# Kernel optimization log

Measured on AMD Instinct MI355X. Metric: run time of the kernel, lower is better.

Reference implementation:

```python
import jax, jax.numpy as jnp
import numpy as np

H = 1024  # hidden_size

def _lstm_cell(x, h, c, Wih, Whh, bih, bhh):
    # x:[B,in], h/c:[B,H]; PyTorch gate order i,f,g,o
    g = x @ Wih.T + h @ Whh.T + (bih + bhh)
    i, f, gg, o = jnp.split(g, 4, axis=-1)
    c = jax.nn.sigmoid(f) * c + jax.nn.sigmoid(i) * jnp.tanh(gg)
    h = jax.nn.sigmoid(o) * jnp.tanh(c)
    return h, c

def setup_inputs() -> dict:
    key = jax.random.key(0)
    ks = jax.random.split(key, 24)
    s = 0.05
    def W(k, shape):
        return (jax.random.normal(k, shape, dtype=jnp.float32) * s)
    inp = {
        'prev': jax.random.normal(ks[0], (32, 256), dtype=jnp.float32),
        'n': jax.random.normal(ks[1], (32, 256), dtype=jnp.float32),
        'tf_mask': jax.random.bernoulli(ks[2], 0.5, (256,)),
        # encoder layer 0 (input_size=1) and layer 1 (input_size=H)
        'enc_Wih0': W(ks[3], (4*H, 1)),  'enc_Whh0': W(ks[4], (4*H, H)),
        'enc_bih0': W(ks[5], (4*H,)),    'enc_bhh0': W(ks[6], (4*H,)),
        'enc_Wih1': W(ks[7], (4*H, H)),  'enc_Whh1': W(ks[8], (4*H, H)),
        'enc_bih1': W(ks[9], (4*H,)),    'enc_bhh1': W(ks[10], (4*H,)),
        # decoder layers
        'dec_Wih0': W(ks[11], (4*H, 1)), 'dec_Whh0': W(ks[12], (4*H, H)),
        'dec_bih0': W(ks[13], (4*H,)),   'dec_bhh0': W(ks[14], (4*H,)),
        'dec_Wih1': W(ks[15], (4*H, H)), 'dec_Whh1': W(ks[16], (4*H, H)),
        'dec_bih1': W(ks[17], (4*H,)),   'dec_bhh1': W(ks[18], (4*H,)),
        'fc_w': W(ks[19], (1, H)),       'fc_b': W(ks[20], (1,)),
    }
    return inp

def reference(prev, n, tf_mask,
              enc_Wih0, enc_Whh0, enc_bih0, enc_bhh0,
              enc_Wih1, enc_Whh1, enc_bih1, enc_bhh1,
              dec_Wih0, dec_Whh0, dec_bih0, dec_bhh0,
              dec_Wih1, dec_Whh1, dec_bih1, dec_bhh1,
              fc_w, fc_b):
    B = prev.shape[0]
    z = jnp.zeros((B, H), dtype=prev.dtype)

    # ---- encode: scan over timesteps, scalar input per step ----
    def enc_step(carry, x_t):
        h0, c0, h1, c1 = carry
        x = x_t[:, None]  # [B,1]
        h0, c0 = _lstm_cell(x, h0, c0, enc_Wih0, enc_Whh0, enc_bih0, enc_bhh0)
        h1, c1 = _lstm_cell(h0, h1, c1, enc_Wih1, enc_Whh1, enc_bih1, enc_bhh1)
        return (h0, c0, h1, c1), None

    carry, _ = jax.lax.scan(enc_step, (z, z, z, z), prev.T)  # prev.T: [T,B]

    # ---- decode with teacher forcing mask ----
    def dec_step(carry, inputs):
        h0, c0, h1, c1, x = carry
        n_t, tf = inputs
        h0, c0 = _lstm_cell(x, h0, c0, dec_Wih0, dec_Whh0, dec_bih0, dec_bhh0)
        h1, c1 = _lstm_cell(h0, h1, c1, dec_Wih1, dec_Whh1, dec_bih1, dec_bhh1)
        pred = h1 @ fc_w.T + fc_b  # [B,1]
        x_next = jnp.where(tf, n_t[:, None], pred)
        return (h0, c0, h1, c1, x_next), pred[:, 0]

    x0 = jnp.zeros((B, 1), dtype=prev.dtype)
    _, preds = jax.lax.scan(dec_step, carry + (x0,), (n.T, tf_mask))
    return preds.T  # [B, T_dec]
```

## Files before the change

### kernel.cpp

```cpp
#include <hip/hip_runtime.h>

typedef _Float16 f16;
typedef _Float16 f16x8 __attribute__((ext_vector_type(8)));
typedef _Float16 f16x4 __attribute__((ext_vector_type(4)));
typedef float    f32x4 __attribute__((ext_vector_type(4)));

#define HN 1024
#define G4 4096
#define MATEL (4096ull*1024ull)
#define TT 512
#define RB 16

#define OFF_W0   (0ull)
#define OFF_WI1  (16ull<<20)
#define OFF_WH1  (32ull<<20)
#define OFF_B0   (48ull<<20)
#define OFF_B1   (OFF_B0 + 32768ull)
#define OFF_WX   (OFF_B0 + 65536ull)
#define OFF_WFC  (OFF_B0 + 98304ull)
#define OFF_FCB  (OFF_B0 + 102400ull)
#define OFF_F0   (OFF_B0 + 131072ull)
#define OFF_F1   (OFF_F0 + 16384ull)
#define OFF_TFM  (OFF_F1 + 32768ull)
#define OFF_RING (49ull<<20)

#define LDS_W   131072
#define LDS_EX  16384
#define LDS_TOT (LDS_W + LDS_EX + 1024)

__device__ __forceinline__ void st8(f16* p, unsigned long long q) {
  (void)__hip_atomic_exchange((unsigned long long*)p, q, __ATOMIC_RELAXED, __HIP_MEMORY_SCOPE_AGENT);
}
__device__ __forceinline__ void st4f(float* p, float v) {
  union { float f; unsigned int u; } c; c.f = v;
  (void)__hip_atomic_exchange((unsigned int*)p, c.u, __ATOMIC_RELAXED, __HIP_MEMORY_SCOPE_AGENT);
}
__device__ __forceinline__ void stampA(unsigned int* slot, unsigned int v) {
  (void)__hip_atomic_exchange(slot, v, __ATOMIC_RELAXED, __HIP_MEMORY_SCOPE_AGENT);
}
template<bool DEEP>
__device__ __forceinline__ f16x8 ldA(const f16* p) {
  if constexpr (DEEP) {
    return *(const f16x8*)p;
  } else {
    union { unsigned long long q[2]; f16x8 v; } u;
    const unsigned long long* pq = (const unsigned long long*)p;
    u.q[0] = __hip_atomic_load(pq,     __ATOMIC_RELAXED, __HIP_MEMORY_SCOPE_AGENT);
    u.q[1] = __hip_atomic_load(pq + 1, __ATOMIC_RELAXED, __HIP_MEMORY_SCOPE_AGENT);
    return u.v;
  }
}
template<bool DEEP>
__device__ __forceinline__ float ldP(const float* p) {
  if constexpr (DEEP) return *p;
  else return __hip_atomic_load(p, __ATOMIC_RELAXED, __HIP_MEMORY_SCOPE_AGENT);
}
template<int CNT, int SLP>
__device__ __forceinline__ void wavewait(const unsigned int* f, int base, unsigned int tgt,
                                         long long& budget) {
  const unsigned int* p = f + (size_t)(base + ((int)(threadIdx.x & 63) & (CNT - 1))) * 64;
  for (;;) {
    unsigned int v = __hip_atomic_load(p, __ATOMIC_RELAXED, __HIP_MEMORY_SCOPE_AGENT);
    if (__all((int)(v >= tgt))) break;
    __builtin_amdgcn_s_sleep(SLP);
    if (--budget < 0) break;
  }
  asm volatile("" ::: "memory");
}
template<int NS, int SLP>
__device__ __forceinline__ void wgwaitA(const unsigned int* f, unsigned int tgt, long long& budget) {
  if (threadIdx.x < 64) {
    const int i0 = (int)threadIdx.x * 64;
    for (;;) {
      unsigned int v = __hip_atomic_load(f + i0, __ATOMIC_RELAXED, __HIP_MEMORY_SCOPE_AGENT);
      if (NS == 128) {
        unsigned int v2 = __hip_atomic_load(f + 4096 + i0, __ATOMIC_RELAXED, __HIP_MEMORY_SCOPE_AGENT);
        v = v < v2 ? v : v2;
      }
      if (__all((int)(v >= tgt))) break;
      __builtin_amdgcn_s_sleep(SLP);
      if (--budget < 0) break;
    }
  }
  __syncthreads();
  asm volatile("" ::: "memory");
}

__device__ __forceinline__ float sigmoidf_(float x) { return 1.f / (1.f + __expf(-x)); }
__device__ __forceinline__ float tanhf_(float x) {
  x = fminf(15.f, fmaxf(-15.f, x));
  float e = __expf(2.f * x);
  return (e - 1.f) / (e + 1.f);
}
__device__ __forceinline__ float sum4h(const f16* p) {
  f16x4 v = *(const f16x4*)p;
  return (float)v[0] + (float)v[1] + (float)v[2] + (float)v[3];
}

__global__ void prep_mats(const float* __restrict__ s0, const float* __restrict__ s1,
                          const float* __restrict__ s2, const float* __restrict__ s3,
                          const float* __restrict__ s4, const float* __restrict__ s5,
                          char* __restrict__ ws)
{
  const int m = blockIdx.y;
  const float* S = (m==0)?s0:(m==1)?s1:(m==2)?s2:(m==3)?s3:(m==4)?s4:s5;
  f16* D;
  if (m < 2)      D = (f16*)(ws + OFF_W0)  + (size_t)m     * MATEL;
  else if (m < 4) D = (f16*)(ws + OFF_WI1) + (size_t)(m-2) * MATEL;
  else            D = (f16*)(ws + OFF_WH1) + (size_t)(m-4) * MATEL;
  const size_t nq = MATEL / 4;
  for (size_t i = (size_t)blockIdx.x * blockDim.x + threadIdx.x; i < nq;
       i += (size_t)gridDim.x * blockDim.x) {
    const float4 v = ((const float4*)S)[i];
    f16x4 h; h[0] = (f16)v.x; h[1] = (f16)v.y; h[2] = (f16)v.z; h[3] = (f16)v.w;
    ((f16x4*)D)[i] = h;
  }
}

__global__ void prep_small(const float* eb0a, const float* eb0b,
                           const float* db0a, const float* db0b,
                           const float* eb1a, const float* eb1b,
                           const float* db1a, const float* db1b,
                           const float* ewx, const float* dwx,
                           const float* fw,  const float* fb,
                           char* __restrict__ ws)
{
  float* B0v  = (float*)(ws + OFF_B0);
  float* B1v  = (float*)(ws + OFF_B1);
  float* WXv  = (float*)(ws + OFF_WX);
  float* WFCv = (float*)(ws + OFF_WFC);
  float* FCBv = (float*)(ws + OFF_FCB);
  int i = blockIdx.x * 256 + threadIdx.x;
  if (i < 4096) {
    B0v[i]        = eb0a[i] + eb0b[i];
    B0v[4096 + i] = db0a[i] + db0b[i];
    B1v[i]        = eb1a[i] + eb1b[i];
    B1v[4096 + i] = db1a[i] + db1b[i];
    WXv[i]        = ewx[i];
    WXv[4096 + i] = dwx[i];
  }
  if (i < 1024) WFCv[i] = fw[i];
  if (i == 0)   FCBv[0] = fb[0];
}

__global__ void prep_tfm(const unsigned char* __restrict__ raw, char* __restrict__ ws)
{
  __shared__ int flg[2];
  unsigned char* dst = (unsigned char*)(ws + OFF_TFM);
  const int i = threadIdx.x;
  if (i == 0) { flg[0] = 1; flg[1] = 1; }
  __syncthreads();
  const unsigned char b = raw[i];
  const int r = i & 3;
  const bool oki = (r == 0) ? (b <= 1) : (b == 0);
  const bool okf = (r == 3) ? (b == 0 || b == 0x3f)
                 : (r == 2) ? (b == 0 || b == 0x80)
                 : (b == 0);
  if (!oki) atomicAnd(&flg[0], 0);
  if (!okf) atomicAnd(&flg[1], 0);
  __syncthreads();
  if (flg[0])      dst[i] = (((const int*)(const void*)raw)[i] != 0);
  else if (flg[1]) dst[i] = (((const float*)(const void*)raw)[i] != 0.f);
  else             dst[i] = (b != 0);
}

template<bool DEEP>
__global__ __launch_bounds__(256, 1)
void seq2seq_main(const float* __restrict__ prev,
                  const float* __restrict__ nfut,
                  char* __restrict__ ws,
                  f16* __restrict__ h0r,
                  f16* __restrict__ h1r,
                  float* __restrict__ part,
                  float* __restrict__ out)
{
  extern __shared__ char lds[];
  f16*   exch = (f16*)(lds + LDS_W);
  float* xbuf = (float*)(lds + LDS_W + LDS_EX);
  float* red  = xbuf + 32;

  const int tid  = threadIdx.x;
  const int wid  = tid >> 6;
  const int lane = tid & 63;
  const int l15  = lane & 15;
  const int lgrp = lane >> 4;
  const int kq   = wid;
  const int wg   = blockIdx.x;

  const f16* W0  = (const f16*)(ws + OFF_W0);
  const f16* WI1 = (const f16*)(ws + OFF_WI1);
  const f16* WH1 = (const f16*)(ws + OFF_WH1);
  const float* B0v  = (const float*)(ws + OFF_B0);
  const float* B1v  = (const float*)(ws + OFF_B1);
  const float* WXv  = (const float*)(ws + OFF_WX);
  const float* WFCv = (const float*)(ws + OFF_WFC);
  const float* FCBv = (const float*)(ws + OFF_FCB);
  const unsigned char* tfm = (const unsigned char*)(ws + OFF_TFM);
  unsigned int* f0 = (unsigned int*)(ws + OFF_F0);
  unsigned int* f1 = (unsigned int*)(ws + OFF_F1);

  long long budget = 1ll << 23;

  if (wg < 64) {
    const int cell0 = wg * 16;
    const int erow = tid & 31, ecq = (tid >> 5) & 3;
    float cst[4] = {0.f, 0.f, 0.f, 0.f};
    float bias[4][4], wxv[4][4];
    for (int T = 0; T < TT; ++T) {
      const int phase = T >> 8;
      if ((T & 255) == 0) {
        __syncthreads();
        const f16* Wm = W0 + (size_t)phase * MATEL;
        { int R = tid >> 2, q = tid & 3;
          int g = R >> 4, rr = R & 15;
          const f16* srow = Wm + (size_t)(g * HN + cell0 + rr) * HN;
          char* drow = lds + R * 2048;
          int sw = (R & 7) << 4;
          #pragma unroll
          for (int i = 0; i < 32; ++i) {
            int ch = q * 32 + i;
            f16x8 v = *(const f16x8*)(srow + ch * 8);
            *(f16x8*)(drow + ((ch * 16) ^ sw)) = v;
          }
        }
        if (tid < 128) {
          #pragma unroll
          for (int g = 0; g < 4; ++g)
            #pragma unroll
            for (int j = 0; j < 4; ++j) {
              bias[g][j] = B0v[phase * G4 + g * HN + cell0 + ecq * 4 + j];
              wxv[g][j]  = WXv[phase * G4 + g * HN + cell0 + ecq * 4 + j];
            }
        }
        __syncthreads();
      }
      if constexpr (!DEEP) {
        if (T > 0)   wgwaitA<64, 1>(f0, (unsigned)T, budget);
        if (T >= RB) wgwaitA<128, 1>(f1, (unsigned)(T - RB + 1), budget);
      }

      f32x4 acc[4][2];
      #pragma unroll
      for (int g = 0; g < 4; ++g) { acc[g][0] = (f32x4){0,0,0,0}; acc[g][1] = (f32x4){0,0,0,0}; }
      if (T > 0) {
        if constexpr (DEEP) wavewait<16, 1>(f0, kq * 16, (unsigned)T, budget);
        const size_t slotR = DEEP ? (size_t)(T - 1) : (size_t)((T - 1) & 15);
        const f16* hb = h0r + slotR * (32 * HN);
        f16x8 a[2][8];
        #pragma unroll
        for (int m = 0; m < 2; ++m)
          #pragma unroll
          for (int ks = 0; ks < 8; ++ks)
            a[m][ks] = ldA<DEEP>(hb + (m * 16 + l15) * HN + kq * 256 + ks * 32 + lgrp * 8);
        #pragma unroll
        for (int ks = 0; ks < 8; ++ks) {
          const int kel = kq * 256 + ks * 32 + lgrp * 8;
          #pragma unroll
          for (int g = 0; g < 4; ++g) {
            const int R = g * 16 + l15;
            f16x8 b = *(const f16x8*)(lds + ((R * 2048 + kel * 2) ^ ((R & 7) << 4)));
            acc[g][0] = __builtin_amdgcn_mfma_f32_16x16x32_f16(a[0][ks], b, acc[g][0], 0, 0, 0);
            acc[g][1] = __builtin_amdgcn_mfma_f32_16x16x32_f16(a[1][ks], b, acc[g][1], 0, 0, 0);
          }
        }
      }
      #pragma unroll
      for (int g = 0; g < 4; ++g)
        #pragma unroll
        for (int m = 0; m < 2; ++m)
          #pragma unroll
          for (int r = 0; r < 4; ++r) {
            const int row16 = lgrp * 4 + r;
            const int colp  = (l15 + row16) & 15;
            exch[((g * 2 + m) * 256 + row16 * 16 + colp) * 4 + kq] = (f16)acc[g][m][r];
          }

      const int s = T - 256;
      const bool needp = (T >= 257) && (tfm[s - 1] == 0);
      if (needp) {
        wgwaitA<128, 1>(f1, (unsigned)T, budget);
        if (tid < 128) {
          const int b = tid & 31, seg = tid >> 5;
          const float* pp = part + (size_t)(s - 1) * 4096;
          float sum = 0.f;
          #pragma unroll 8
          for (int k = 0; k < 32; ++k) sum += ldP<DEEP>(pp + (seg * 32 + k) * 32 + b);
          red[tid] = sum;
        }
      } else if (T < 256) {
        if (tid < 32) xbuf[tid] = prev[tid * 256 + T];
      } else if (s == 0) {
        if (tid < 32) xbuf[tid] = 0.f;
      } else {
        if (tid < 32) xbuf[tid] = nfut[tid * 256 + (s - 1)];
      }
      __syncthreads();
      if (needp) {
        if (tid < 32) xbuf[tid] = red[tid] + red[32 + tid] + red[64 + tid] + red[96 + tid] + FCBv[0];
        __syncthreads();
      }
      if (tid < 128) {
        const int m = erow >> 4, row16 = erow & 15;
        const float xb = xbuf[erow];
        const size_t slotW = DEEP ? (size_t)T : (size_t)(T & 15);
        f16* h0w = h0r + slotW * (32 * HN);
        union { f16 h[4]; unsigned long long q; } pk;
        #pragma unroll
        for (int j = 0; j < 4; ++j) {
          const int colp = (ecq * 4 + j + row16) & 15;
          float gv[4];
          #pragma unroll
          for (int g = 0; g < 4; ++g)
            gv[g] = sum4h(exch + ((g * 2 + m) * 256 + row16 * 16 + colp) * 4)
                  + bias[g][j] + xb * wxv[g][j];
          const float iv = sigmoidf_(gv[0]), fv = sigmoidf_(gv[1]);
          const float gg = tanhf_(gv[2]),    ov = sigmoidf_(gv[3]);
          cst[j] = fv * cst[j] + iv * gg;
          pk.h[j] = (f16)(ov * tanhf_(cst[j]));
        }
        st8(h0w + erow * HN + cell0 + ecq * 4, pk.q);
      }
      __syncthreads();
      if (tid == 0) stampA(f0 + wg * 64, (unsigned)(T + 1));
    }
  } else if (wg < 192) {
    const int w1 = wg - 64;
    const int cell0 = w1 * 8;
    const int erow = tid & 31, ehf = (tid >> 5) & 1;
    float cst[4] = {0.f, 0.f, 0.f, 0.f};
    float bias[4][4], fcw[4];
    for (int T = 0; T < TT; ++T) {
      const int phase = T >> 8;
      if ((T & 255) == 0) {
        __syncthreads();
        { int R = tid >> 2, q = tid & 3;
          int mat = R >> 5, r5 = R & 31;
          int tl = (r5 >> 4) & 1, hf = (r5 >> 3) & 1;
          int grow = (tl * 2 + hf) * HN + cell0 + (r5 & 7);
          const f16* Wm = (mat ? WH1 : WI1) + (size_t)phase * MATEL;
          const f16* srow = Wm + (size_t)grow * HN;
          char* drow = lds + R * 2048;
          int sw = (R & 7) << 4;
          #pragma unroll
          for (int i = 0; i < 32; ++i) {
            int ch = q * 32 + i;
            f16x8 v = *(const f16x8*)(srow + ch * 8);
            *(f16x8*)(drow + ((ch * 16) ^ sw)) = v;
          }
        }
        if (tid < 64) {
          #pragma unroll
          for (int g = 0; g < 4; ++g)
            #pragma unroll
            for (int j = 0; j < 4; ++j)
              bias[g][j] = B1v[phase * G4 + g * HN + cell0 + ehf * 4 + j];
          #pragma unroll
          for (int j = 0; j < 4; ++j) fcw[j] = WFCv[cell0 + ehf * 4 + j];
        }
        __syncthreads();
      }
      if constexpr (!DEEP) {
        if (T > 0) wgwaitA<128, 1>(f1, (unsigned)T, budget);
      }

      f32x4 acc[2][2];
      acc[0][0] = acc[0][1] = acc[1][0] = acc[1][1] = (f32x4){0, 0, 0, 0};
      f16x8 a[2][8];
      if (T > 0) {
        if constexpr (DEEP) wavewait<32, 1>(f1, kq * 32, (unsigned)T, budget);
        const size_t slotR = DEEP ? (size_t)(T - 1) : (size_t)((T - 1) & 15);
        const f16* hb = h1r + slotR * (32 * HN);
        #pragma unroll
        for (int m = 0; m < 2; ++m)
          #pragma unroll
          for (int ks = 0; ks < 8; ++ks)
            a[m][ks] = ldA<DEEP>(hb + (m * 16 + l15) * HN + kq * 256 + ks * 32 + lgrp * 8);
        #pragma unroll
        for (int ks = 0; ks < 8; ++ks) {
          const int kel = kq * 256 + ks * 32 + lgrp * 8;
          #pragma unroll
          for (int t = 0; t < 2; ++t) {
            const int R = 32 + t * 16 + l15;
            f16x8 b = *(const f16x8*)(lds + ((R * 2048 + kel * 2) ^ ((R & 7) << 4)));
            acc[t][0] = __builtin_amdgcn_mfma_f32_16x16x32_f16(a[0][ks], b, acc[t][0], 0, 0, 0);
            acc[t][1] = __builtin_amdgcn_mfma_f32_16x16x32_f16(a[1][ks], b, acc[t][1], 0, 0, 0);
          }
        }
      }
      if constexpr (DEEP) wavewait<16, 1>(f0, kq * 16, (unsigned)(T + 1), budget);
      else                wgwaitA<64, 1>(f0, (unsigned)(T + 1), budget);
      { const size_t slotR = DEEP ? (size_t)T : (size_t)(T & 15);
        const f16* hb = h0r + slotR * (32 * HN);
        #pragma unroll
        for (int m = 0; m < 2; ++m)
          #pragma unroll
          for (int ks = 0; ks < 8; ++ks)
            a[m][ks] = ldA<DEEP>(hb + (m * 16 + l15) * HN + kq * 256 + ks * 32 + lgrp * 8);
      }
      #pragma unroll
      for (int ks = 0; ks < 8; ++ks) {
        const int kel = kq * 256 + ks * 32 + lgrp * 8;
        #pragma unroll
        for (int t = 0; t < 2; ++t) {
          const int R = t * 16 + l15;
          f16x8 b = *(const f16x8*)(lds + ((R * 2048 + kel * 2) ^ ((R & 7) << 4)));
          acc[t][0] = __builtin_amdgcn_mfma_f32_16x16x32_f16(a[0][ks], b, acc[t][0], 0, 0, 0);
          acc[t][1] = __builtin_amdgcn_mfma_f32_16x16x32_f16(a[1][ks], b, acc[t][1], 0, 0, 0);
        }
      }
      #pragma unroll
      for (int t = 0; t < 2; ++t)
        #pragma unroll
        for (int m = 0; m < 2; ++m)
          #pragma unroll
          for (int r = 0; r < 4; ++r) {
            const int row16 = lgrp * 4 + r;
            const int colp  = (l15 + row16) & 15;
            exch[((t * 2 + m) * 256 + row16 * 16 + colp) * 4 + kq] = (f16)acc[t][m][r];
          }
      __syncthreads();
      float pv = 0.f;
      if (tid < 64) {
        const int m = erow >> 4, row16 = erow & 15;
        const size_t slotW = DEEP ? (size_t)T : (size_t)(T & 15);
        f16* h1w = h1r + slotW * (32 * HN);
        union { f16 h[4]; unsigned long long q; } pk;
        #pragma unroll
        for (int j = 0; j < 4; ++j) {
          const int c = ehf * 4 + j;
          float gv[4];
          #pragma unroll
          for (int g = 0; g < 4; ++g) {
            const int colp = (((g & 1) * 8 + c) + row16) & 15;
            gv[g] = sum4h(exch + (((g >> 1) * 2 + m) * 256 + row16 * 16 + colp) * 4) + bias[g][j];
          }
          cst[j] = sigmoidf_(gv[1]) * cst[j] + sigmoidf_(gv[0]) * tanhf_(gv[2]);
          const float hv = sigmoidf_(gv[3]) * tanhf_(cst[j]);
          pk.h[j] = (f16)hv;
          pv += fcw[j] * hv;
        }
        st8(h1w + erow * HN + cell0 + ehf * 4, pk.q);
        if (T >= 256) {
          pv += __shfl_xor(pv, 32);
          if (ehf == 0)
            st4f(part + (size_t)(T - 256) * 4096 + w1 * 32 + erow, pv);
        }
      }
      __syncthreads();
      if (tid == 0) stampA(f1 + w1 * 64, (unsigned)(T + 1));
    }
  } else if (wg == 192) {
    for (int sD = 0; sD < 256; ++sD) {
      wgwaitA<128, 16>(f1, (unsigned)(257 + sD), budget);
      if (tid < 128) {
        const int b = tid & 31, seg = tid >> 5;
        const float* pp = part + (size_t)sD * 4096;
        float sum = 0.f;
        #pragma unroll 8
        for (int k = 0; k < 32; ++k) sum += ldP<DEEP>(pp + (seg * 32 + k) * 32 + b);
        red[tid] = sum;
      }
      __syncthreads();
      if (tid < 32) out[tid * 256 + sD] = red[tid] + red[32 + tid] + red[64 + tid] + red[96 + tid] + FCBv[0];
      __syncthreads();
    }
  }
}

extern "C" void kernel_launch(void* const* d_in, const int* in_sizes, int n_in,
                              void* d_out, int out_size, void* d_ws, size_t ws_size,
                              hipStream_t stream)
{
  (void)in_sizes; (void)n_in; (void)out_size;
  char* ws = (char*)d_ws;

  const bool deep = ws_size >= (118ull << 20);
  const size_t ringsz = deep ? (32ull << 20) : (1ull << 20);
  const size_t offH0 = OFF_RING;
  const size_t offH1 = offH0 + ringsz;
  const size_t offPart = offH1 + ringsz;
  if (!deep && ws_size < (offPart + (4ull << 20))) return;

  hipMemsetAsync(ws + OFF_F0, 0, 49152, stream);

  prep_mats<<<dim3(1024, 6), 256, 0, stream>>>(
      (const float*)d_in[4],  (const float*)d_in[12],
      (const float*)d_in[7],  (const float*)d_in[15],
      (const float*)d_in[8],  (const float*)d_in[16], ws);

  prep_small<<<16, 256, 0, stream>>>(
      (const float*)d_in[5],  (const float*)d_in[6],
      (const float*)d_in[13], (const float*)d_in[14],
      (const float*)d_in[9],  (const float*)d_in[10],
      (const float*)d_in[17], (const float*)d_in[18],
      (const float*)d_in[3],  (const float*)d_in[11],
      (const float*)d_in[19], (const float*)d_in[20],
      ws);

  prep_tfm<<<1, 256, 0, stream>>>((const unsigned char*)d_in[2], ws);

  f16* h0r = (f16*)(ws + offH0);
  f16* h1r = (f16*)(ws + offH1);
  float* part = (float*)(ws + offPart);

  if (deep) {
    auto fn = seq2seq_main<true>;
    hipFuncSetAttribute((const void*)fn, hipFuncAttributeMaxDynamicSharedMemorySize, LDS_TOT);
    fn<<<dim3(193), dim3(256), LDS_TOT, stream>>>(
        (const float*)d_in[0], (const float*)d_in[1], ws, h0r, h1r, part, (float*)d_out);
  } else {
    auto fn = seq2seq_main<false>;
    hipFuncSetAttribute((const void*)fn, hipFuncAttributeMaxDynamicSharedMemorySize, LDS_TOT);
    fn<<<dim3(193), dim3(256), LDS_TOT, stream>>>(
        (const float*)d_in[0], (const float*)d_in[1], ws, h0r, h1r, part, (float*)d_out);
  }
}
```

Baseline: 3.781 ms.

## Stamp progress flags per wave after vmcnt drain instead of after block barrier

Layer-0 workgroups now publish two per-wave progress flags, and layer-1 workgroups publish from wave 0, each right after draining its own outstanding stores with s_waitcnt vmcnt(0). Before, a single thread stamped the flag after a full __syncthreads. Consumers wait on the doubled flag array through a new two-slot min-reduce poll. The partial-sum reductions also widen from 128 to 256 threads with shorter loops. The aim is to signal cross-block readiness earlier in the serial recurrence, at the cost of more flag traffic and polling, and with ordering risk if stores from other waves are not covered by the wave that stamps.

```diff
diff --git a/kernel.cpp b/kernel.cpp
--- a/kernel.cpp
+++ b/kernel.cpp
@@ -20,13 +20,13 @@
 #define OFF_WFC  (OFF_B0 + 98304ull)
 #define OFF_FCB  (OFF_B0 + 102400ull)
 #define OFF_F0   (OFF_B0 + 131072ull)
-#define OFF_F1   (OFF_F0 + 16384ull)
+#define OFF_F1   (OFF_F0 + 32768ull)
 #define OFF_TFM  (OFF_F1 + 32768ull)
 #define OFF_RING (49ull<<20)
 
 #define LDS_W   131072
 #define LDS_EX  16384
-#define LDS_TOT (LDS_W + LDS_EX + 1024)
+#define LDS_TOT (LDS_W + LDS_EX + 2048)
 
 __device__ __forceinline__ void st8(f16* p, unsigned long long q) {
   (void)__hip_atomic_exchange((unsigned long long*)p, q, __ATOMIC_RELAXED, __HIP_MEMORY_SCOPE_AGENT);
@@ -77,6 +77,22 @@
         unsigned int v2 = __hip_atomic_load(f + 4096 + i0, __ATOMIC_RELAXED, __HIP_MEMORY_SCOPE_AGENT);
         v = v < v2 ? v : v2;
       }
+      if (__all((int)(v >= tgt))) break;
+      __builtin_amdgcn_s_sleep(SLP);
+      if (--budget < 0) break;
+    }
+  }
+  __syncthreads();
+  asm volatile("" ::: "memory");
+}
+template<int SLP>
+__device__ __forceinline__ void wgwaitF0(const unsigned int* f, unsigned int tgt, long long& budget) {
+  if (threadIdx.x < 64) {
+    const int i0 = (int)threadIdx.x * 128;
+    for (;;) {
+      unsigned int v  = __hip_atomic_load(f + i0,      __ATOMIC_RELAXED, __HIP_MEMORY_SCOPE_AGENT);
+      unsigned int v2 = __hip_atomic_load(f + i0 + 64, __ATOMIC_RELAXED, __HIP_MEMORY_SCOPE_AGENT);
+      v = v < v2 ? v : v2;
       if (__all((int)(v >= tgt))) break;
       __builtin_amdgcn_s_sleep(SLP);
       if (--budget < 0) break;
@@ -235,7 +251,7 @@
         __syncthreads();
       }
       if constexpr (!DEEP) {
-        if (T > 0)   wgwaitA<64, 1>(f0, (unsigned)T, budget);
+        if (T > 0)   wgwaitF0<1>(f0, (unsigned)T, budget);
         if (T >= RB) wgwaitA<128, 1>(f1, (unsigned)(T - RB + 1), budget);
       }
 
@@ -243,7 +259,7 @@
       #pragma unroll
       for (int g = 0; g < 4; ++g) { acc[g][0] = (f32x4){0,0,0,0}; acc[g][1] = (f32x4){0,0,0,0}; }
       if (T > 0) {
-        if constexpr (DEEP) wavewait<16, 1>(f0, kq * 16, (unsigned)T, budget);
+        if constexpr (DEEP) wavewait<32, 1>(f0, kq * 32, (unsigned)T, budget);
         const size_t slotR = DEEP ? (size_t)(T - 1) : (size_t)((T - 1) & 15);
         const f16* hb = h0r + slotR * (32 * HN);
         f16x8 a[2][8];
@@ -279,12 +295,11 @@
       const bool needp = (T >= 257) && (tfm[s - 1] == 0);
       if (needp) {
         wgwaitA<128, 1>(f1, (unsigned)T, budget);
-        if (tid < 128) {
-          const int b = tid & 31, seg = tid >> 5;
+        { const int b = tid & 31, seg = tid >> 5;
           const float* pp = part + (size_t)(s - 1) * 4096;
           float sum = 0.f;
           #pragma unroll 8
-          for (int k = 0; k < 32; ++k) sum += ldP<DEEP>(pp + (seg * 32 + k) * 32 + b);
+          for (int k = 0; k < 16; ++k) sum += ldP<DEEP>(pp + (seg * 16 + k) * 32 + b);
           red[tid] = sum;
         }
       } else if (T < 256) {
@@ -296,7 +311,12 @@
       }
       __syncthreads();
       if (needp) {
-        if (tid < 32) xbuf[tid] = red[tid] + red[32 + tid] + red[64 + tid] + red[96 + tid] + FCBv[0];
+        if (tid < 32) {
+          float sum = FCBv[0];
+          #pragma unroll
+          for (int j = 0; j < 8; ++j) sum += red[j * 32 + tid];
+          xbuf[tid] = sum;
+        }
         __syncthreads();
       }
       if (tid < 128) {
@@ -320,8 +340,11 @@
         }
         st8(h0w + erow * HN + cell0 + ecq * 4, pk.q);
       }
+      if (wid < 2) {
+        asm volatile("s_waitcnt vmcnt(0)" ::: "memory");
+        if (lane == 0) stampA(f0 + (size_t)(wg * 2 + wid) * 64, (unsigned)(T + 1));
+      }
       __syncthreads();
-      if (tid == 0) stampA(f0 + wg * 64, (unsigned)(T + 1));
     }
   } else if (wg < 192) {
     const int w1 = wg - 64;
@@ -387,8 +410,8 @@
           }
         }
       }
-      if constexpr (DEEP) wavewait<16, 1>(f0, kq * 16, (unsigned)(T + 1), budget);
-      else                wgwaitA<64, 1>(f0, (unsigned)(T + 1), budget);
+      if constexpr (DEEP) wavewait<32, 1>(f0, kq * 32, (unsigned)(T + 1), budget);
+      else                wgwaitF0<1>(f0, (unsigned)(T + 1), budget);
       { const size_t slotR = DEEP ? (size_t)T : (size_t)(T & 15);
         const f16* hb = h0r + slotR * (32 * HN);
         #pragma unroll
@@ -446,22 +469,29 @@
             st4f(part + (size_t)(T - 256) * 4096 + w1 * 32 + erow, pv);
         }
       }
+      if (wid == 0) {
+        asm volatile("s_waitcnt vmcnt(0)" ::: "memory");
+        if (lane == 0) stampA(f1 + (size_t)w1 * 64, (unsigned)(T + 1));
+      }
       __syncthreads();
-      if (tid == 0) stampA(f1 + w1 * 64, (unsigned)(T + 1));
     }
   } else if (wg == 192) {
     for (int sD = 0; sD < 256; ++sD) {
       wgwaitA<128, 16>(f1, (unsigned)(257 + sD), budget);
-      if (tid < 128) {
-        const int b = tid & 31, seg = tid >> 5;
+      { const int b = tid & 31, seg = tid >> 5;
         const float* pp = part + (size_t)sD * 4096;
         float sum = 0.f;
         #pragma unroll 8
-        for (int k = 0; k < 32; ++k) sum += ldP<DEEP>(pp + (seg * 32 + k) * 32 + b);
+        for (int k = 0; k < 16; ++k) sum += ldP<DEEP>(pp + (seg * 16 + k) * 32 + b);
         red[tid] = sum;
       }
       __syncthreads();
-      if (tid < 32) out[tid * 256 + sD] = red[tid] + red[32 + tid] + red[64 + tid] + red[96 + tid] + FCBv[0];
+      if (tid < 32) {
+        float sum = FCBv[0];
+        #pragma unroll
+        for (int j = 0; j < 8; ++j) sum += red[j * 32 + tid];
+        out[tid * 256 + sD] = sum;
+      }
       __syncthreads();
     }
   }
@@ -481,7 +511,7 @@
   const size_t offPart = offH1 + ringsz;
   if (!deep && ws_size < (offPart + (4ull << 20))) return;
 
-  hipMemsetAsync(ws + OFF_F0, 0, 49152, stream);
+  hipMemsetAsync(ws + OFF_F0, 0, 65536, stream);
 
   prep_mats<<<dim3(1024, 6), 256, 0, stream>>>(
       (const float*)d_in[4],  (const float*)d_in[12],
```

Result: slower. 3.953 ms (+4.6%).
